# Optimization experiments

Hardware: AMD Instinct MI355X
Metric: run time of the kernel (lower is better)

Reference implementation:

```python
import jax, jax.numpy as jnp
import numpy as np
import math

B, LA, LB, D, H = 8, 2048, 2048, 512, 512

def setup_inputs() -> dict:
    key = jax.random.key(0)
    ks = jax.random.split(key, 6)
    return {
        "input_a": jax.random.normal(ks[0], (B, LA, D), dtype=jnp.float32),
        "input_b": jax.random.normal(ks[1], (B, LB, D), dtype=jnp.float32),
        "mask_a": jax.random.randint(ks[2], (B, LA), 0, 2, dtype=jnp.int32),
        "mask_b": jax.random.randint(ks[3], (B, LB), 0, 2, dtype=jnp.int32),
        "Wa": jax.random.normal(ks[4], (D, H), dtype=jnp.float32) * (1.0 / math.sqrt(D)),
        "ba": jnp.zeros((H,), dtype=jnp.float32),
        "Wb": jax.random.normal(ks[5], (D, H), dtype=jnp.float32) * (1.0 / math.sqrt(D)),
        "bb": jnp.zeros((H,), dtype=jnp.float32),
    }

def reference(input_a, input_b, mask_a, mask_b, Wa, ba, Wb, bb):
    scale = 1.0 / math.sqrt(D)  # math.sqrt(input_dim_a)
    mapped_a = input_a @ Wa + ba            # [B, La, H]
    mapped_b = input_b @ Wb + bb            # [B, Lb, H]
    # final_mask = (mask_a outer mask_b) == 0
    final_mask = (mask_a[:, :, None] * mask_b[:, None, :]) == 0  # [B, La, Lb]
    scores = jnp.einsum('bih,bjh->bij', mapped_a, mapped_b) * scale
    scores = jnp.where(final_mask, jnp.float32(-1e9), scores)
    # attentions_a = softmax over Lb; attentions_b^T = softmax over La axis
    att_a = jax.nn.softmax(scores, axis=-1)   # [B, La, Lb]
    att_bT = jax.nn.softmax(scores, axis=1)   # [B, La, Lb] (= attentions_b.transpose(1,2))
    output_a = jnp.einsum('bij,bjd->bid', att_bT, input_b)  # [B, La, D]
    output_b = jnp.einsum('bij,bid->bjd', att_a, input_a)   # [B, Lb, D]
    return (output_a + input_a, output_b + input_b)
```

## Files before the change

### kernel.cpp

```cpp
#include <hip/hip_runtime.h>
#include <hip/hip_bf16.h>

#define BATCH 8
#define LSEQ 2048
#define DDIM 512

using f32x4 = __attribute__((ext_vector_type(4))) float;
using s16x8 = __attribute__((ext_vector_type(8))) short;
using s16x4 = __attribute__((ext_vector_type(4))) short;

static __device__ __forceinline__ unsigned short f2b(float f) {
  __hip_bfloat16 h = __float2bfloat16(f);
  return __builtin_bit_cast(unsigned short, h);
}
static __device__ __forceinline__ float b2f(unsigned short u) {
  unsigned int v = ((unsigned int)u) << 16;
  return __builtin_bit_cast(float, v);
}

static __device__ __forceinline__ void gld16(const unsigned short* g, unsigned short* l) {
  __builtin_amdgcn_global_load_lds(
      (__attribute__((address_space(1))) void*)(g),
      (__attribute__((address_space(3))) void*)(l), 16, 0, 0);
}

__device__ __forceinline__ void mfma_kloop(
    const unsigned short* __restrict__ A, const unsigned short* __restrict__ Bt,
    int K, int lda, int ldb, unsigned short* sA, unsigned short* sB,
    int tid, f32x4 acc[4][4]) {
  const int wave = tid >> 6, lane = tid & 63;
  const int wm = (wave >> 1) * 64, wn = (wave & 1) * 64;
  const int lr = lane & 15, lq = lane >> 4;
  const int srow = tid >> 2;
  const int sk = (tid & 3) * 8;
  unsigned short* dA0 = sA + wave * 512;
  unsigned short* dA1 = sA + 2048 + wave * 512;
  unsigned short* dB0 = sB + wave * 512;
  unsigned short* dB1 = sB + 2048 + wave * 512;
  const unsigned short* pa0 = A + (size_t)srow * lda + sk;
  const unsigned short* pa1 = A + (size_t)(srow + 64) * lda + sk;
  const unsigned short* pb0 = Bt + (size_t)srow * ldb + sk;
  const unsigned short* pb1 = Bt + (size_t)(srow + 64) * ldb + sk;
  for (int k0 = 0; k0 < K; k0 += 32) {
    gld16(pa0 + k0, dA0);
    gld16(pa1 + k0, dA1);
    gld16(pb0 + k0, dB0);
    gld16(pb1 + k0, dB1);
    __syncthreads();
    s16x8 af[4], bf[4];
#pragma unroll
    for (int r = 0; r < 4; ++r)
      af[r] = *(const s16x8*)(sA + (wm + r * 16 + lr) * 32 + lq * 8);
#pragma unroll
    for (int c = 0; c < 4; ++c)
      bf[c] = *(const s16x8*)(sB + (wn + c * 16 + lr) * 32 + lq * 8);
#pragma unroll
    for (int r = 0; r < 4; ++r)
#pragma unroll
      for (int c = 0; c < 4; ++c)
        acc[r][c] = __builtin_amdgcn_mfma_f32_16x16x32_bf16(af[r], bf[c], acc[r][c], 0, 0, 0);
    __syncthreads();
  }
}

__global__ __launch_bounds__(256) void k_prep(const float* __restrict__ in_a,
                                              const float* __restrict__ in_b,
                                              const int* __restrict__ ma,
                                              const int* __restrict__ mb,
                                              unsigned short* __restrict__ oa,
                                              unsigned short* __restrict__ ob,
                                              float* __restrict__ Pa,
                                              float* __restrict__ Pb) {
  int z = blockIdx.z;
  const float* in = z ? in_b : in_a;
  const int* mask = z ? mb : ma;
  unsigned short* o16 = z ? ob : oa;
  float* partial = z ? Pb : Pa;
  int b = blockIdx.y;
  int l0 = blockIdx.x * 32;
  __shared__ int sm[32];
  if (threadIdx.x < 32) sm[threadIdx.x] = mask[b * LSEQ + l0 + threadIdx.x];
  __syncthreads();
  int d = threadIdx.x * 2;
  const float* base = in + ((size_t)b * LSEQ + l0) * DDIM + d;
  unsigned short* obase = o16 + ((size_t)b * LSEQ + l0) * DDIM + d;
  float ax = 0.f, ay = 0.f;
#pragma unroll 4
  for (int r = 0; r < 32; ++r) {
    float2 v = *(const float2*)(base + (size_t)r * DDIM);
    ushort2 u; u.x = f2b(v.x); u.y = f2b(v.y);
    *(ushort2*)(obase + (size_t)r * DDIM) = u;
    if (sm[r] == 0) { ax += v.x; ay += v.y; }
  }
  float2 o; o.x = ax; o.y = ay;
  *(float2*)(partial + ((size_t)(b * 64 + blockIdx.x)) * DDIM + d) = o;
}

__global__ __launch_bounds__(256) void k_p2(const float* __restrict__ Pa,
                                            const float* __restrict__ Pb,
                                            float* __restrict__ Ca,
                                            float* __restrict__ Cb) {
  int g = blockIdx.x;
  const float* src = (g < 8) ? Pa : Pb;
  float* dst = (g < 8) ? Ca : Cb;
  int b = g & 7;
  int d = threadIdx.x * 2;
  float ax = 0.f, ay = 0.f;
  for (int c = 0; c < 64; ++c) {
    float2 v = *(const float2*)(src + ((size_t)(b * 64 + c)) * DDIM + d);
    ax += v.x; ay += v.y;
  }
  dst[b * DDIM + d] = ax * (1.0f / LSEQ);
  dst[b * DDIM + d + 1] = ay * (1.0f / LSEQ);
}

__global__ __launch_bounds__(256) void k_transposeW(const float* __restrict__ Wa,
                                                    const float* __restrict__ Wb,
                                                    unsigned short* __restrict__ WaT,
                                                    unsigned short* __restrict__ WbT) {
  int gidx = blockIdx.x * 256 + threadIdx.x;
  const float* W = (gidx < 512 * 512) ? Wa : Wb;
  unsigned short* WT = (gidx < 512 * 512) ? WaT : WbT;
  int idx = gidx & (512 * 512 - 1);
  int h = idx >> 9, d = idx & 511;
  WT[idx] = f2b(W[d * DDIM + h]);
}

__global__ __launch_bounds__(256) void k_gemm_bias(const unsigned short* __restrict__ a16,
                                                   const unsigned short* __restrict__ b16,
                                                   const unsigned short* __restrict__ WaT,
                                                   const unsigned short* __restrict__ WbT,
                                                   const float* __restrict__ ba,
                                                   const float* __restrict__ bb,
                                                   unsigned short* __restrict__ mapa,
                                                   unsigned short* __restrict__ mapb) {
  int id = blockIdx.x;
  int g = id >> 5, rem = id & 31;
  int bn = (rem >> 3) * 128;
  int f = g * 8 + (rem & 7);
  int bm = (f & 127) * 128;
  int z = f >> 7;
  const unsigned short* A = z ? b16 : a16;
  const unsigned short* Bt = z ? WbT : WaT;
  const float* bias = z ? bb : ba;
  unsigned short* Cout = z ? mapb : mapa;
  __shared__ __align__(16) unsigned short sA[128 * 32], sB[128 * 32];
  f32x4 acc[4][4];
  f32x4 zero = {0.f, 0.f, 0.f, 0.f};
#pragma unroll
  for (int r = 0; r < 4; ++r)
#pragma unroll
    for (int c = 0; c < 4; ++c) acc[r][c] = zero;
  mfma_kloop(A + (size_t)bm * DDIM, Bt + (size_t)bn * DDIM, DDIM, DDIM, DDIM,
             sA, sB, threadIdx.x, acc);
  int wave = threadIdx.x >> 6, lane = threadIdx.x & 63;
  int wm = (wave >> 1) * 64, wn = (wave & 1) * 64, lr = lane & 15, lq = lane >> 4;
#pragma unroll
  for (int r = 0; r < 4; ++r)
#pragma unroll
    for (int c = 0; c < 4; ++c)
#pragma unroll
      for (int rr = 0; rr < 4; ++rr) {
        int row = bm + wm + r * 16 + lq * 4 + rr;
        int col = bn + wn + c * 16 + lr;
        Cout[(size_t)row * DDIM + col] = f2b(acc[r][c][rr] + bias[col]);
      }
}

__global__ __launch_bounds__(512, 2) void k_scores(
    const unsigned short* __restrict__ mapa, const unsigned short* __restrict__ mapb,
    const int* __restrict__ mask_a, const int* __restrict__ mask_b,
    unsigned short* __restrict__ E, unsigned short* __restrict__ Et,
    float* __restrict__ Zrow, float* __restrict__ Zcol) {
  int w = (blockIdx.x & 7) * 64 + (blockIdx.x >> 3);
  int b = w >> 6, t = w & 63;
  int bi = (t >> 3) * 256, bj = (t & 7) * 256;
  const unsigned short* Aop = mapa + ((size_t)b * LSEQ + bi) * DDIM;
  const unsigned short* Bop = mapb + ((size_t)b * LSEQ + bj) * DDIM;

  __shared__ __align__(16) unsigned short smem[65536];
  unsigned short* sA = smem;
  unsigned short* sB = smem + 32768;
  __shared__ int sMa[256], sMb[256];

  const int tid = threadIdx.x;
  const int wave = tid >> 6, lane = tid & 63;
  const int wr = wave >> 2, wc = wave & 3;
  const int lr = lane & 15, lq = lane >> 4;

  const int srow = tid >> 2;
  const int kcsw = ((tid & 3) ^ (srow & 3)) * 8;
  const unsigned short* pa0 = Aop + (size_t)srow * DDIM + kcsw;
  const unsigned short* pa1 = pa0 + (size_t)128 * DDIM;
  const unsigned short* pb0 = Bop + (size_t)srow * DDIM + kcsw;
  const unsigned short* pb1 = pb0 + (size_t)128 * DDIM;
  unsigned short* dA = sA + wave * 512;
  unsigned short* dB = sB + wave * 512;

  int aoff[8], boff[4];
#pragma unroll
  for (int m = 0; m < 8; ++m)
    aoff[m] = (wr * 128 + m * 16 + lr) * 32 + (lq ^ (lr & 3)) * 8;
#pragma unroll
  for (int n = 0; n < 4; ++n)
    boff[n] = (wc * 64 + n * 16 + lr) * 32 + (lq ^ (lr & 3)) * 8;

  f32x4 acc[8][4];
  f32x4 zero = {0.f, 0.f, 0.f, 0.f};
#pragma unroll
  for (int m = 0; m < 8; ++m)
#pragma unroll
    for (int n = 0; n < 4; ++n) acc[m][n] = zero;

#define SGA(c) { const int sl_ = ((c) & 3) * 8192; \
  gld16(pa0 + (size_t)(c) * 32, dA + sl_); \
  gld16(pa1 + (size_t)(c) * 32, dA + sl_ + 4096); }
#define SGB(c) { const int sl_ = ((c) & 3) * 8192; \
  gld16(pb0 + (size_t)(c) * 32, dB + sl_); \
  gld16(pb1 + (size_t)(c) * 32, dB + sl_ + 4096); }

  SGA(0); SGB(0); SGA(1); SGB(1); SGA(2); SGB(2);
  asm volatile("s_waitcnt vmcnt(8)\ns_barrier" ::: "memory");

  for (int j = 0; j < 16; ++j) {
    const int sl = (j & 3) * 8192;
    s16x8 af[8];
#pragma unroll
    for (int m = 0; m < 8; ++m) af[m] = *(const s16x8*)(sA + sl + aoff[m]);
    s16x8 bf0 = *(const s16x8*)(sB + sl + boff[0]);
    s16x8 bf1 = *(const s16x8*)(sB + sl + boff[1]);
    if (j < 13) SGA(j + 3);
    __builtin_amdgcn_s_setprio(1);
#pragma unroll
    for (int m = 0; m < 8; ++m) {
      acc[m][0] = __builtin_amdgcn_mfma_f32_16x16x32_bf16(af[m], bf0, acc[m][0], 0, 0, 0);
      acc[m][1] = __builtin_amdgcn_mfma_f32_16x16x32_bf16(af[m], bf1, acc[m][1], 0, 0, 0);
    }
    __builtin_amdgcn_s_setprio(0);
    asm volatile("s_barrier" ::: "memory");
    s16x8 bf2 = *(const s16x8*)(sB + sl + boff[2]);
    s16x8 bf3 = *(const s16x8*)(sB + sl + boff[3]);
    if (j < 13) SGB(j + 3);
    __builtin_amdgcn_s_setprio(1);
#pragma unroll
    for (int m = 0; m < 8; ++m) {
      acc[m][2] = __builtin_amdgcn_mfma_f32_16x16x32_bf16(af[m], bf2, acc[m][2], 0, 0, 0);
      acc[m][3] = __builtin_amdgcn_mfma_f32_16x16x32_bf16(af[m], bf3, acc[m][3], 0, 0, 0);
    }
    __builtin_amdgcn_s_setprio(0);
    if (j < 13)
      asm volatile("s_waitcnt vmcnt(8)\ns_barrier" ::: "memory");
    else if (j == 13)
      asm volatile("s_waitcnt vmcnt(4)\ns_barrier" ::: "memory");
    else
      asm volatile("s_waitcnt vmcnt(0)\ns_barrier" ::: "memory");
  }
#undef SGA
#undef SGB

  if (tid < 256)
    sMa[tid] = mask_a[b * LSEQ + bi + tid];
  else
    sMb[tid - 256] = mask_b[b * LSEQ + bj + tid - 256];
  __syncthreads();

  const float scale = 0.044194173824159216f;
  unsigned short* Eb = E + (size_t)b * LSEQ * LSEQ + (size_t)bi * LSEQ + bj;
  float rowp[8][4];
  float colp[4] = {0.f, 0.f, 0.f, 0.f};
#pragma unroll
  for (int m = 0; m < 8; ++m) {
#pragma unroll
    for (int rr = 0; rr < 4; ++rr) rowp[m][rr] = 0.f;
#pragma unroll
    for (int n = 0; n < 4; ++n) {
      int jl = wc * 64 + n * 16 + lr;
      int mb_ = sMb[jl];
      s16x4 tq;
#pragma unroll
      for (int rr = 0; rr < 4; ++rr) {
        int il = wr * 128 + m * 16 + lq * 4 + rr;
        float e = (sMa[il] && mb_) ? __expf(acc[m][n][rr] * scale) : 0.f;
        rowp[m][rr] += e;
        colp[n] += e;
        unsigned short eb = f2b(e);
        tq[rr] = (short)eb;
        Eb[(size_t)il * LSEQ + jl] = eb;
      }
      int il0 = wr * 128 + m * 16 + lq * 4;
      *(s16x4*)(smem + jl * 256 + (il0 ^ ((jl & 7) << 3))) = tq;
    }
  }
#pragma unroll
  for (int m = 0; m < 8; ++m)
#pragma unroll
    for (int rr = 0; rr < 4; ++rr) {
      float v = rowp[m][rr];
      v += __shfl_xor(v, 1);
      v += __shfl_xor(v, 2);
      v += __shfl_xor(v, 4);
      v += __shfl_xor(v, 8);
      if (lr == 0) {
        int il = wr * 128 + m * 16 + lq * 4 + rr;
        atomicAdd(&Zrow[b * LSEQ + bi + il], v);
      }
    }
#pragma unroll
  for (int n = 0; n < 4; ++n) {
    float v = colp[n];
    v += __shfl_xor(v, 16);
    v += __shfl_xor(v, 32);
    if (lq == 0) atomicAdd(&Zcol[b * LSEQ + bj + wc * 64 + n * 16 + lr], v);
  }
  __syncthreads();
  unsigned short* EtB = Et + (size_t)b * LSEQ * LSEQ + (size_t)bj * LSEQ + bi;
#pragma unroll
  for (int p = 0; p < 16; ++p) {
    int idx = p * 512 + tid;
    int jlr = idx >> 5, chk = idx & 31;
    s16x8 v = *(const s16x8*)(smem + jlr * 256 + ((chk * 8) ^ ((jlr & 7) << 3)));
    *(s16x8*)(EtB + (size_t)jlr * LSEQ + chk * 8) = v;
  }
}

__global__ __launch_bounds__(256) void k_scaleT(const unsigned short* __restrict__ a16,
                                                const unsigned short* __restrict__ b16,
                                                const float* __restrict__ Zrow,
                                                const float* __restrict__ Zcol,
                                                unsigned short* __restrict__ atS,
                                                unsigned short* __restrict__ btS) {
  int zz = blockIdx.z;
  int b = zz & 7, sel = zz >> 3;
  const unsigned short* in = sel ? b16 : a16;
  const float* Z = sel ? Zcol : Zrow;
  unsigned short* out = sel ? btS : atS;
  int i0 = blockIdx.y * 64, d0 = blockIdx.x * 64;
  __shared__ unsigned short lt[64 * 65];
  __shared__ float zinv[64];
  if (threadIdx.x < 64) {
    float z = Z[b * LSEQ + i0 + threadIdx.x];
    zinv[threadIdx.x] = (z > 0.f) ? 1.f / z : 0.f;
  }
  __syncthreads();
  const unsigned short* ib = in + ((size_t)b * LSEQ + i0) * DDIM + d0;
#pragma unroll
  for (int p = 0; p < 16; ++p) {
    int idx = p * 256 + threadIdx.x;
    int dl = idx & 63, il = idx >> 6;
    lt[dl * 65 + il] = f2b(b2f(ib[(size_t)il * DDIM + dl]) * zinv[il]);
  }
  __syncthreads();
  unsigned short* ob = out + ((size_t)b * DDIM + d0) * LSEQ + i0;
#pragma unroll
  for (int p = 0; p < 16; ++p) {
    int idx = p * 256 + threadIdx.x;
    int il = idx & 63, dl = idx >> 6;
    ob[(size_t)dl * LSEQ + il] = lt[dl * 65 + il];
  }
}

__global__ __launch_bounds__(512, 2) void k_gemm_outs(
    const unsigned short* __restrict__ E, const unsigned short* __restrict__ Et,
    const unsigned short* __restrict__ btS, const unsigned short* __restrict__ atS,
    const unsigned short* __restrict__ a16, const unsigned short* __restrict__ b16,
    const float* __restrict__ Ca, const float* __restrict__ Cb,
    float* __restrict__ OutA, float* __restrict__ OutB) {
  int w = (blockIdx.x & 7) * 32 + (blockIdx.x >> 3);
  int mode = w >> 7;
  int r0 = w & 127;
  int b = r0 >> 4, tile = r0 & 15;
  int bm = (tile >> 1) * 256, bn = (tile & 1) * 256;
  const unsigned short* Aop = (mode ? Et : E) + (size_t)b * LSEQ * LSEQ + (size_t)bm * LSEQ;
  const unsigned short* Bop = (mode ? atS : btS) + (size_t)b * DDIM * LSEQ + (size_t)bn * LSEQ;
  const unsigned short* addin = mode ? b16 : a16;
  const float* Cvec = mode ? Ca : Cb;
  float* Out = mode ? OutB : OutA;

  __shared__ __align__(16) unsigned short sA[4 * 8192], sB[4 * 8192];
  const int tid = threadIdx.x;
  const int wave = tid >> 6, lane = tid & 63;
  const int wr = wave >> 2, wc = wave & 3;
  const int lr = lane & 15, lq = lane >> 4;

  const int srow = tid >> 2;
  const int kcsw = ((tid & 3) ^ (srow & 3)) * 8;
  const unsigned short* pa0 = Aop + (size_t)srow * LSEQ + kcsw;
  const unsigned short* pa1 = pa0 + (size_t)128 * LSEQ;
  const unsigned short* pb0 = Bop + (size_t)srow * LSEQ + kcsw;
  const unsigned short* pb1 = pb0 + (size_t)128 * LSEQ;
  unsigned short* dA = sA + wave * 512;
  unsigned short* dB = sB + wave * 512;

  int aoff[8], boff[4];
#pragma unroll
  for (int m = 0; m < 8; ++m)
    aoff[m] = (wr * 128 + m * 16 + lr) * 32 + (lq ^ (lr & 3)) * 8;
#pragma unroll
  for (int n = 0; n < 4; ++n)
    boff[n] = (wc * 64 + n * 16 + lr) * 32 + (lq ^ (lr & 3)) * 8;

  f32x4 acc[8][4];
  f32x4 zero = {0.f, 0.f, 0.f, 0.f};
#pragma unroll
  for (int m = 0; m < 8; ++m)
#pragma unroll
    for (int n = 0; n < 4; ++n) acc[m][n] = zero;

#define SGA(c) { const int sl_ = ((c) & 3) * 8192; \
  gld16(pa0 + (size_t)(c) * 32, dA + sl_); \
  gld16(pa1 + (size_t)(c) * 32, dA + sl_ + 4096); }
#define SGB(c) { const int sl_ = ((c) & 3) * 8192; \
  gld16(pb0 + (size_t)(c) * 32, dB + sl_); \
  gld16(pb1 + (size_t)(c) * 32, dB + sl_ + 4096); }

  SGA(0); SGB(0); SGA(1); SGB(1); SGA(2); SGB(2);
  asm volatile("s_waitcnt vmcnt(8)\ns_barrier" ::: "memory");

  for (int j = 0; j < 64; ++j) {
    const int sl = (j & 3) * 8192;
    s16x8 af[8];
#pragma unroll
    for (int m = 0; m < 8; ++m) af[m] = *(const s16x8*)(sA + sl + aoff[m]);
    s16x8 bf0 = *(const s16x8*)(sB + sl + boff[0]);
    s16x8 bf1 = *(const s16x8*)(sB + sl + boff[1]);
    if (j < 61) SGA(j + 3);
    __builtin_amdgcn_s_setprio(1);
#pragma unroll
    for (int m = 0; m < 8; ++m) {
      acc[m][0] = __builtin_amdgcn_mfma_f32_16x16x32_bf16(af[m], bf0, acc[m][0], 0, 0, 0);
      acc[m][1] = __builtin_amdgcn_mfma_f32_16x16x32_bf16(af[m], bf1, acc[m][1], 0, 0, 0);
    }
    __builtin_amdgcn_s_setprio(0);
    asm volatile("s_barrier" ::: "memory");
    s16x8 bf2 = *(const s16x8*)(sB + sl + boff[2]);
    s16x8 bf3 = *(const s16x8*)(sB + sl + boff[3]);
    if (j < 61) SGB(j + 3);
    __builtin_amdgcn_s_setprio(1);
#pragma unroll
    for (int m = 0; m < 8; ++m) {
      acc[m][2] = __builtin_amdgcn_mfma_f32_16x16x32_bf16(af[m], bf2, acc[m][2], 0, 0, 0);
      acc[m][3] = __builtin_amdgcn_mfma_f32_16x16x32_bf16(af[m], bf3, acc[m][3], 0, 0, 0);
    }
    __builtin_amdgcn_s_setprio(0);
    if (j < 61)
      asm volatile("s_waitcnt vmcnt(8)\ns_barrier" ::: "memory");
    else if (j == 61)
      asm volatile("s_waitcnt vmcnt(4)\ns_barrier" ::: "memory");
    else
      asm volatile("s_waitcnt vmcnt(0)\ns_barrier" ::: "memory");
  }
#undef SGA
#undef SGB

#pragma unroll
  for (int m = 0; m < 8; ++m)
#pragma unroll
    for (int n = 0; n < 4; ++n)
#pragma unroll
      for (int rr = 0; rr < 4; ++rr) {
        int row = bm + wr * 128 + m * 16 + lq * 4 + rr;
        int col = bn + wc * 64 + n * 16 + lr;
        size_t o = ((size_t)b * LSEQ + row) * DDIM + col;
        Out[o] = acc[m][n][rr] + b2f(addin[o]) + Cvec[b * DDIM + col];
      }
}

extern "C" void kernel_launch(void* const* d_in, const int* in_sizes, int n_in,
                              void* d_out, int out_size, void* d_ws, size_t ws_size,
                              hipStream_t stream) {
  (void)in_sizes; (void)n_in; (void)out_size; (void)ws_size;
  const float* in_a = (const float*)d_in[0];
  const float* in_b = (const float*)d_in[1];
  const int* ma = (const int*)d_in[2];
  const int* mb = (const int*)d_in[3];
  const float* Wa = (const float*)d_in[4];
  const float* ba = (const float*)d_in[5];
  const float* Wb = (const float*)d_in[6];
  const float* bb = (const float*)d_in[7];
  float* out = (float*)d_out;

  char* ws = (char*)d_ws;
  const size_t MB = 1ull << 20;
  unsigned short* a16 = (unsigned short*)(ws + 0 * MB);
  unsigned short* b16 = (unsigned short*)(ws + 16 * MB);
  unsigned short* WaT = (unsigned short*)(ws + 32 * MB);
  unsigned short* WbT = (unsigned short*)(ws + 32 * MB + 512 * 1024);
  unsigned short* mapa = (unsigned short*)(ws + 33 * MB);
  unsigned short* mapb = (unsigned short*)(ws + 49 * MB);
  unsigned short* E = (unsigned short*)(ws + 65 * MB);
  unsigned short* atS = (unsigned short*)(ws + 129 * MB);
  unsigned short* btS = (unsigned short*)(ws + 145 * MB);
  float* Zrow = (float*)(ws + 161 * MB);
  float* Zcol = (float*)(ws + 161 * MB + 65536);
  float* Ca = (float*)(ws + 161 * MB + 2 * 65536);
  float* Cb = (float*)(ws + 161 * MB + 2 * 65536 + 16384);
  float* Pa = (float*)(ws + 162 * MB);
  float* Pb = (float*)(ws + 163 * MB);
  unsigned short* Et = (unsigned short*)(ws + 164 * MB);

  hipMemsetAsync(Zrow, 0, 2 * 65536, stream);
  k_prep<<<dim3(64, 8, 2), 256, 0, stream>>>(in_a, in_b, ma, mb, a16, b16, Pa, Pb);
  k_transposeW<<<2048, 256, 0, stream>>>(Wa, Wb, WaT, WbT);
  k_p2<<<16, 256, 0, stream>>>(Pa, Pb, Ca, Cb);
  k_gemm_bias<<<1024, 256, 0, stream>>>(a16, b16, WaT, WbT, ba, bb, mapa, mapb);
  k_scores<<<512, 512, 0, stream>>>(mapa, mapb, ma, mb, E, Et, Zrow, Zcol);
  k_scaleT<<<dim3(8, 32, 16), 256, 0, stream>>>(a16, b16, Zrow, Zcol, atS, btS);
  k_gemm_outs<<<256, 512, 0, stream>>>(E, Et, btS, atS, a16, b16, Ca, Cb,
                                       out, out + (size_t)BATCH * LSEQ * DDIM);
}
```

Baseline: 330.4 us.

## Pipeline projection GEMM with 256x256 tiles and fold column-sum reduction into atomics

The projection GEMM moves from 128x128 tiles with a synchronous two-barrier k-loop to 256x256 tiles on 512 threads. It uses a 4-stage global_load_lds ring buffer, XOR-swizzled LDS addressing, split MFMA phases with setprio, and an XCD-aware block remap. This is meant to hide load latency and raise operand reuse. Separately, the second-pass reduction kernel k_p2 is removed: k_prep now atomically adds scaled partial sums into Ca/Cb, which are zeroed by the existing memset. That saves a launch at the cost of atomic contention and a nondeterministic summation order.

```diff
diff --git a/kernel.cpp b/kernel.cpp
--- a/kernel.cpp
+++ b/kernel.cpp
@@ -22,45 +22,6 @@
   __builtin_amdgcn_global_load_lds(
       (__attribute__((address_space(1))) void*)(g),
       (__attribute__((address_space(3))) void*)(l), 16, 0, 0);
-}
-
-__device__ __forceinline__ void mfma_kloop(
-    const unsigned short* __restrict__ A, const unsigned short* __restrict__ Bt,
-    int K, int lda, int ldb, unsigned short* sA, unsigned short* sB,
-    int tid, f32x4 acc[4][4]) {
-  const int wave = tid >> 6, lane = tid & 63;
-  const int wm = (wave >> 1) * 64, wn = (wave & 1) * 64;
-  const int lr = lane & 15, lq = lane >> 4;
-  const int srow = tid >> 2;
-  const int sk = (tid & 3) * 8;
-  unsigned short* dA0 = sA + wave * 512;
-  unsigned short* dA1 = sA + 2048 + wave * 512;
-  unsigned short* dB0 = sB + wave * 512;
-  unsigned short* dB1 = sB + 2048 + wave * 512;
-  const unsigned short* pa0 = A + (size_t)srow * lda + sk;
-  const unsigned short* pa1 = A + (size_t)(srow + 64) * lda + sk;
-  const unsigned short* pb0 = Bt + (size_t)srow * ldb + sk;
-  const unsigned short* pb1 = Bt + (size_t)(srow + 64) * ldb + sk;
-  for (int k0 = 0; k0 < K; k0 += 32) {
-    gld16(pa0 + k0, dA0);
-    gld16(pa1 + k0, dA1);
-    gld16(pb0 + k0, dB0);
-    gld16(pb1 + k0, dB1);
-    __syncthreads();
-    s16x8 af[4], bf[4];
-#pragma unroll
-    for (int r = 0; r < 4; ++r)
-      af[r] = *(const s16x8*)(sA + (wm + r * 16 + lr) * 32 + lq * 8);
-#pragma unroll
-    for (int c = 0; c < 4; ++c)
-      bf[c] = *(const s16x8*)(sB + (wn + c * 16 + lr) * 32 + lq * 8);
-#pragma unroll
-    for (int r = 0; r < 4; ++r)
-#pragma unroll
-      for (int c = 0; c < 4; ++c)
-        acc[r][c] = __builtin_amdgcn_mfma_f32_16x16x32_bf16(af[r], bf[c], acc[r][c], 0, 0, 0);
-    __syncthreads();
-  }
 }
 
 __global__ __launch_bounds__(256) void k_prep(const float* __restrict__ in_a,
@@ -69,13 +30,13 @@
                                               const int* __restrict__ mb,
                                               unsigned short* __restrict__ oa,
                                               unsigned short* __restrict__ ob,
-                                              float* __restrict__ Pa,
-                                              float* __restrict__ Pb) {
+                                              float* __restrict__ Ca,
+                                              float* __restrict__ Cb) {
   int z = blockIdx.z;
   const float* in = z ? in_b : in_a;
   const int* mask = z ? mb : ma;
   unsigned short* o16 = z ? ob : oa;
-  float* partial = z ? Pb : Pa;
+  float* cdst = z ? Cb : Ca;
   int b = blockIdx.y;
   int l0 = blockIdx.x * 32;
   __shared__ int sm[32];
@@ -92,26 +53,10 @@
     *(ushort2*)(obase + (size_t)r * DDIM) = u;
     if (sm[r] == 0) { ax += v.x; ay += v.y; }
   }
-  float2 o; o.x = ax; o.y = ay;
-  *(float2*)(partial + ((size_t)(b * 64 + blockIdx.x)) * DDIM + d) = o;
-}
-
-__global__ __launch_bounds__(256) void k_p2(const float* __restrict__ Pa,
-                                            const float* __restrict__ Pb,
-                                            float* __restrict__ Ca,
-                                            float* __restrict__ Cb) {
-  int g = blockIdx.x;
-  const float* src = (g < 8) ? Pa : Pb;
-  float* dst = (g < 8) ? Ca : Cb;
-  int b = g & 7;
-  int d = threadIdx.x * 2;
-  float ax = 0.f, ay = 0.f;
-  for (int c = 0; c < 64; ++c) {
-    float2 v = *(const float2*)(src + ((size_t)(b * 64 + c)) * DDIM + d);
-    ax += v.x; ay += v.y;
-  }
-  dst[b * DDIM + d] = ax * (1.0f / LSEQ);
-  dst[b * DDIM + d + 1] = ay * (1.0f / LSEQ);
+  if (ax != 0.f || ay != 0.f || true) {
+    atomicAdd(&cdst[b * DDIM + d], ax * (1.0f / LSEQ));
+    atomicAdd(&cdst[b * DDIM + d + 1], ay * (1.0f / LSEQ));
+  }
 }
 
 __global__ __launch_bounds__(256) void k_transposeW(const float* __restrict__ Wa,
@@ -126,44 +71,108 @@
   WT[idx] = f2b(W[d * DDIM + h]);
 }
 
-__global__ __launch_bounds__(256) void k_gemm_bias(const unsigned short* __restrict__ a16,
-                                                   const unsigned short* __restrict__ b16,
-                                                   const unsigned short* __restrict__ WaT,
-                                                   const unsigned short* __restrict__ WbT,
-                                                   const float* __restrict__ ba,
-                                                   const float* __restrict__ bb,
-                                                   unsigned short* __restrict__ mapa,
-                                                   unsigned short* __restrict__ mapb) {
-  int id = blockIdx.x;
-  int g = id >> 5, rem = id & 31;
-  int bn = (rem >> 3) * 128;
-  int f = g * 8 + (rem & 7);
-  int bm = (f & 127) * 128;
-  int z = f >> 7;
-  const unsigned short* A = z ? b16 : a16;
-  const unsigned short* Bt = z ? WbT : WaT;
+__global__ __launch_bounds__(512, 2) void k_gemm_bias(
+    const unsigned short* __restrict__ a16, const unsigned short* __restrict__ b16,
+    const unsigned short* __restrict__ WaT, const unsigned short* __restrict__ WbT,
+    const float* __restrict__ ba, const float* __restrict__ bb,
+    unsigned short* __restrict__ mapa, unsigned short* __restrict__ mapb) {
+  int w = (blockIdx.x & 7) * 32 + (blockIdx.x >> 3);
+  int z = w >> 7;
+  int id = w & 127;
+  int bmt = id >> 1;
+  int bn = (id & 1) * 256;
+  int b = bmt >> 3;
+  int row0 = (bmt & 7) * 256;
+  const unsigned short* Aop = (z ? b16 : a16) + ((size_t)b * LSEQ + row0) * DDIM;
+  const unsigned short* Bop = (z ? WbT : WaT) + (size_t)bn * DDIM;
   const float* bias = z ? bb : ba;
-  unsigned short* Cout = z ? mapb : mapa;
-  __shared__ __align__(16) unsigned short sA[128 * 32], sB[128 * 32];
-  f32x4 acc[4][4];
+  unsigned short* Cout = (z ? mapb : mapa) + ((size_t)b * LSEQ + row0) * DDIM;
+
+  __shared__ __align__(16) unsigned short sA[4 * 8192], sB[4 * 8192];
+  const int tid = threadIdx.x;
+  const int wave = tid >> 6, lane = tid & 63;
+  const int wr = wave >> 2, wc = wave & 3;
+  const int lr = lane & 15, lq = lane >> 4;
+
+  const int srow = tid >> 2;
+  const int kcsw = ((tid & 3) ^ (srow & 3)) * 8;
+  const unsigned short* pa0 = Aop + (size_t)srow * DDIM + kcsw;
+  const unsigned short* pa1 = pa0 + (size_t)128 * DDIM;
+  const unsigned short* pb0 = Bop + (size_t)srow * DDIM + kcsw;
+  const unsigned short* pb1 = pb0 + (size_t)128 * DDIM;
+  unsigned short* dA = sA + wave * 512;
+  unsigned short* dB = sB + wave * 512;
+
+  int aoff[8], boff[4];
+#pragma unroll
+  for (int m = 0; m < 8; ++m)
+    aoff[m] = (wr * 128 + m * 16 + lr) * 32 + (lq ^ (lr & 3)) * 8;
+#pragma unroll
+  for (int n = 0; n < 4; ++n)
+    boff[n] = (wc * 64 + n * 16 + lr) * 32 + (lq ^ (lr & 3)) * 8;
+
+  f32x4 acc[8][4];
   f32x4 zero = {0.f, 0.f, 0.f, 0.f};
 #pragma unroll
-  for (int r = 0; r < 4; ++r)
-#pragma unroll
-    for (int c = 0; c < 4; ++c) acc[r][c] = zero;
-  mfma_kloop(A + (size_t)bm * DDIM, Bt + (size_t)bn * DDIM, DDIM, DDIM, DDIM,
-             sA, sB, threadIdx.x, acc);
-  int wave = threadIdx.x >> 6, lane = threadIdx.x & 63;
-  int wm = (wave >> 1) * 64, wn = (wave & 1) * 64, lr = lane & 15, lq = lane >> 4;
-#pragma unroll
-  for (int r = 0; r < 4; ++r)
-#pragma unroll
-    for (int c = 0; c < 4; ++c)
+  for (int m = 0; m < 8; ++m)
+#pragma unroll
+    for (int n = 0; n < 4; ++n) acc[m][n] = zero;
+
+#define SGA(c) { const int sl_ = ((c) & 3) * 8192; \
+  gld16(pa0 + (size_t)(c) * 32, dA + sl_); \
+  gld16(pa1 + (size_t)(c) * 32, dA + sl_ + 4096); }
+#define SGB(c) { const int sl_ = ((c) & 3) * 8192; \
+  gld16(pb0 + (size_t)(c) * 32, dB + sl_); \
+  gld16(pb1 + (size_t)(c) * 32, dB + sl_ + 4096); }
+
+  SGA(0); SGB(0); SGA(1); SGB(1); SGA(2); SGB(2);
+  asm volatile("s_waitcnt vmcnt(8)\ns_barrier" ::: "memory");
+
+  for (int j = 0; j < 16; ++j) {
+    const int sl = (j & 3) * 8192;
+    s16x8 af[8];
+#pragma unroll
+    for (int m = 0; m < 8; ++m) af[m] = *(const s16x8*)(sA + sl + aoff[m]);
+    s16x8 bf0 = *(const s16x8*)(sB + sl + boff[0]);
+    s16x8 bf1 = *(const s16x8*)(sB + sl + boff[1]);
+    if (j < 13) SGA(j + 3);
+    __builtin_amdgcn_s_setprio(1);
+#pragma unroll
+    for (int m = 0; m < 8; ++m) {
+      acc[m][0] = __builtin_amdgcn_mfma_f32_16x16x32_bf16(af[m], bf0, acc[m][0], 0, 0, 0);
+      acc[m][1] = __builtin_amdgcn_mfma_f32_16x16x32_bf16(af[m], bf1, acc[m][1], 0, 0, 0);
+    }
+    __builtin_amdgcn_s_setprio(0);
+    asm volatile("s_barrier" ::: "memory");
+    s16x8 bf2 = *(const s16x8*)(sB + sl + boff[2]);
+    s16x8 bf3 = *(const s16x8*)(sB + sl + boff[3]);
+    if (j < 13) SGB(j + 3);
+    __builtin_amdgcn_s_setprio(1);
+#pragma unroll
+    for (int m = 0; m < 8; ++m) {
+      acc[m][2] = __builtin_amdgcn_mfma_f32_16x16x32_bf16(af[m], bf2, acc[m][2], 0, 0, 0);
+      acc[m][3] = __builtin_amdgcn_mfma_f32_16x16x32_bf16(af[m], bf3, acc[m][3], 0, 0, 0);
+    }
+    __builtin_amdgcn_s_setprio(0);
+    if (j < 13)
+      asm volatile("s_waitcnt vmcnt(8)\ns_barrier" ::: "memory");
+    else if (j == 13)
+      asm volatile("s_waitcnt vmcnt(4)\ns_barrier" ::: "memory");
+    else
+      asm volatile("s_waitcnt vmcnt(0)\ns_barrier" ::: "memory");
+  }
+#undef SGA
+#undef SGB
+
+#pragma unroll
+  for (int m = 0; m < 8; ++m)
+#pragma unroll
+    for (int n = 0; n < 4; ++n)
 #pragma unroll
       for (int rr = 0; rr < 4; ++rr) {
-        int row = bm + wm + r * 16 + lq * 4 + rr;
-        int col = bn + wn + c * 16 + lr;
-        Cout[(size_t)row * DDIM + col] = f2b(acc[r][c][rr] + bias[col]);
+        int row = wr * 128 + m * 16 + lq * 4 + rr;
+        int col = bn + wc * 64 + n * 16 + lr;
+        Cout[(size_t)row * DDIM + col] = f2b(acc[m][n][rr] + bias[col]);
       }
 }
 
@@ -494,15 +503,12 @@
   float* Zcol = (float*)(ws + 161 * MB + 65536);
   float* Ca = (float*)(ws + 161 * MB + 2 * 65536);
   float* Cb = (float*)(ws + 161 * MB + 2 * 65536 + 16384);
-  float* Pa = (float*)(ws + 162 * MB);
-  float* Pb = (float*)(ws + 163 * MB);
   unsigned short* Et = (unsigned short*)(ws + 164 * MB);
 
-  hipMemsetAsync(Zrow, 0, 2 * 65536, stream);
-  k_prep<<<dim3(64, 8, 2), 256, 0, stream>>>(in_a, in_b, ma, mb, a16, b16, Pa, Pb);
+  hipMemsetAsync(Zrow, 0, 2 * 65536 + 2 * 16384, stream);
+  k_prep<<<dim3(64, 8, 2), 256, 0, stream>>>(in_a, in_b, ma, mb, a16, b16, Ca, Cb);
   k_transposeW<<<2048, 256, 0, stream>>>(Wa, Wb, WaT, WbT);
-  k_p2<<<16, 256, 0, stream>>>(Pa, Pb, Ca, Cb);
-  k_gemm_bias<<<1024, 256, 0, stream>>>(a16, b16, WaT, WbT, ba, bb, mapa, mapb);
+  k_gemm_bias<<<256, 512, 0, stream>>>(a16, b16, WaT, WbT, ba, bb, mapa, mapb);
   k_scores<<<512, 512, 0, stream>>>(mapa, mapb, ma, mb, E, Et, Zrow, Zcol);
   k_scaleT<<<dim3(8, 32, 16), 256, 0, stream>>>(a16, b16, Zrow, Zcol, atS, btS);
   k_gemm_outs<<<256, 512, 0, stream>>>(E, Et, btS, atS, a16, b16, Ca, Cb,
```

After: 318.6 us. 1.04x faster.
